# Kernel optimization log

Measured on AMD Instinct MI355X. Metric: run time of the kernel, lower is better.

## Reference

```python
import jax, jax.numpy as jnp
import numpy as np

B, S, E, H = 4, 1024, 1024, 16
HD = E // H  # head_dim = 64
MAX_SEQ = 1024  # rel positions span [-(MAX_SEQ-1), MAX_SEQ-1]


def setup_inputs() -> dict:
    key = jax.random.key(0)
    ks = jax.random.split(key, 12)
    std_e = 1.0 / np.sqrt(E)
    std_h = 1.0 / np.sqrt(HD)
    inp = {
        "x": jax.random.normal(ks[0], (B, S, E), dtype=jnp.float32),
        # torch nn.Linear weights are [out, in]; y = x @ W.T + b
        "Wq": jax.random.uniform(ks[1], (E, E), jnp.float32, -std_e, std_e),
        "bq": jax.random.uniform(ks[2], (E,), jnp.float32, -std_e, std_e),
        "Wk": jax.random.uniform(ks[3], (E, E), jnp.float32, -std_e, std_e),
        "bk": jax.random.uniform(ks[4], (E,), jnp.float32, -std_e, std_e),
        "Wv": jax.random.uniform(ks[5], (E, E), jnp.float32, -std_e, std_e),
        "bv": jax.random.uniform(ks[6], (E,), jnp.float32, -std_e, std_e),
        "Wo": jax.random.uniform(ks[7], (E, E), jnp.float32, -std_e, std_e),
        "bo": jax.random.uniform(ks[8], (E,), jnp.float32, -std_e, std_e),
        # pos_key_proj: Linear(head_dim, head_dim, bias=False)
        "Wp": jax.random.uniform(ks[9], (HD, HD), jnp.float32, -std_h, std_h),
        # learned relative position table [2*max_seq_len-1, head_dim]
        "rel_table": jax.random.normal(ks[10], (2 * MAX_SEQ - 1, HD), dtype=jnp.float32),
    }
    return inp


def _rel_shift(pos_scores):
    # pos_scores: [B, H, S, 2S-1] -> [B, H, S, S]
    # result[..., i, j] = pos_scores[..., i, (S-1) - i + j]
    s = pos_scores.shape[-2]
    idx = (s - 1) - jnp.arange(s)[:, None] + jnp.arange(s)[None, :]  # [S, S]
    return jnp.take_along_axis(pos_scores, idx[None, None, :, :], axis=-1)


def reference(x, Wq, bq, Wk, bk, Wv, bv, Wo, bo, Wp, rel_table):
    scale = 1.0 / np.sqrt(HD)
    Q = (x @ Wq.T + bq).reshape(B, S, H, HD).transpose(0, 2, 1, 3)  # [B,H,S,HD]
    K = (x @ Wk.T + bk).reshape(B, S, H, HD).transpose(0, 2, 1, 3)
    V = (x @ Wv.T + bv).reshape(B, S, H, HD).transpose(0, 2, 1, 3)

    # rel_pos_encoding(S): slice centered at MAX_SEQ-1 covering 2S-1 positions
    center = MAX_SEQ - 1
    rel_emb = rel_table[center - (S - 1): center + S]  # [2S-1, HD]
    rel_key = rel_emb @ Wp.T                            # [2S-1, HD]

    content = jnp.einsum("bhqd,bhkd->bhqk", Q, K) * scale       # [B,H,S,S]
    pos = jnp.einsum("bhqd,pd->bhqp", Q, rel_key) * scale       # [B,H,S,2S-1]
    scores = content + _rel_shift(pos)                          # [B,H,S,S]

    probs = jax.nn.softmax(scores, axis=-1)
    ctx = jnp.einsum("bhqk,bhkd->bhqd", probs, V)               # [B,H,S,HD]
    ctx = ctx.transpose(0, 2, 1, 3).reshape(B, S, E)
    return ctx @ Wo.T + bo
```

## Files before the change

### kernel.cpp

```cpp
#include <hip/hip_runtime.h>
#include <hip/hip_bf16.h>

#define B_   4
#define S_   1024
#define E_   1024
#define H_   16
#define HD_  64

typedef float  f32x4  __attribute__((ext_vector_type(4)));
typedef short  bf16x8 __attribute__((ext_vector_type(8)));
typedef short  bf16x4 __attribute__((ext_vector_type(4)));

__device__ __forceinline__ float bf2f(short u) {
  union { unsigned int i; float f; } v;
  v.i = ((unsigned int)(unsigned short)u) << 16;
  return v.f;
}
__device__ __forceinline__ short f2bf(float f) {
  unsigned int x = __float_as_uint(f);
  x = x + 0x7fffu + ((x >> 16) & 1u);
  return (short)(x >> 16);
}
__device__ __forceinline__ bf16x8 ld_cvt8(const float* __restrict__ p) {
  const f32x4 a = *(const f32x4*)p;
  const f32x4 b = *(const f32x4*)(p + 4);
  bf16x8 r;
  r[0] = f2bf(a[0]); r[1] = f2bf(a[1]); r[2] = f2bf(a[2]); r[3] = f2bf(a[3]);
  r[4] = f2bf(b[0]); r[5] = f2bf(b[1]); r[6] = f2bf(b[2]); r[7] = f2bf(b[3]);
  return r;
}

__device__ __forceinline__ void gload_lds16(const short* g, short* l) {
  __builtin_amdgcn_global_load_lds(
      (const __attribute__((address_space(1))) void*)g,
      (__attribute__((address_space(3))) void*)l, 16, 0, 0);
}

__global__ __launch_bounds__(256) void cvt_f32_bf16(
    const float* __restrict__ src, short* __restrict__ dst, int n)
{
  const int i = (blockIdx.x * 256 + threadIdx.x) * 4;
  if (i < n) {
    const f32x4 v = *(const f32x4*)(src + i);
    bf16x4 o;
    o[0] = f2bf(v[0]); o[1] = f2bf(v[1]); o[2] = f2bf(v[2]); o[3] = f2bf(v[3]);
    *(bf16x4*)(dst + i) = o;
  }
}

__global__ __launch_bounds__(256) void cvt3_f32_bf16(
    const float* __restrict__ s0, const float* __restrict__ s1,
    const float* __restrict__ s2, short* __restrict__ dst, int n)
{
  const float* src = (blockIdx.z == 0) ? s0 : (blockIdx.z == 1) ? s1 : s2;
  short* d = dst + (size_t)blockIdx.z * n;
  const int i = (blockIdx.x * 256 + threadIdx.x) * 4;
  if (i < n) {
    const f32x4 v = *(const f32x4*)(src + i);
    bf16x4 o;
    o[0] = f2bf(v[0]); o[1] = f2bf(v[1]); o[2] = f2bf(v[2]); o[3] = f2bf(v[3]);
    *(bf16x4*)(d + i) = o;
  }
}

template<int TM, int AF32, int OUTF32>
__global__ __launch_bounds__(256) void gemm_bt(
    const void* __restrict__ Av,
    const short* __restrict__ W0, const short* __restrict__ W1, const short* __restrict__ W2,
    const float* __restrict__ b0, const float* __restrict__ b1, const float* __restrict__ b2,
    void* __restrict__ C0v, void* __restrict__ C1v, void* __restrict__ C2v, int vz)
{
  constexpr int NJ = (TM == 128) ? 4 : 2;
  __shared__ short As[TM * 32];
  __shared__ short Bs[128 * 32];

  const int tid  = threadIdx.x;
  const int lane = tid & 63;
  const int wave = tid >> 6;
  const int quad = lane >> 4;
  const int l15  = lane & 15;
  const int wmb  = (TM == 128) ? (wave >> 1) * 64 : 0;
  const int wnb  = (TM == 128) ? (wave & 1) * 64 : wave * 32;
  const int m0   = blockIdx.y * TM;
  const int n0   = blockIdx.x * 128;
  const int z    = blockIdx.z;

  const short* W  = (z == 0) ? W0 : (z == 1) ? W1 : W2;
  const float* bb = (z == 0) ? b0 : (z == 1) ? b1 : b2;
  void*        Cv = (z == 0) ? C0v : (z == 1) ? C1v : C2v;

  const int trow = tid >> 2;
  const int tc   = tid & 3;

  f32x4 acc[4][NJ] = {};

  for (int k0 = 0; k0 < E_; k0 += 32) {
    if (AF32) {
      const float* A = (const float*)Av;
#pragma unroll
      for (int n = 0; n < TM / 64; ++n) {
        const int row = trow + n * 64;
        const int pc  = tc ^ ((row >> 1) & 3);
        *(bf16x8*)&As[row * 32 + pc * 8] = ld_cvt8(A + (size_t)(m0 + row) * E_ + k0 + tc * 8);
      }
    } else {
      const short* A = (const short*)Av;
#pragma unroll
      for (int n = 0; n < TM / 64; ++n) {
        const int row  = trow + n * 64;
        const int srcc = tc ^ ((row >> 1) & 3);
        gload_lds16(A + (size_t)(m0 + row) * E_ + k0 + srcc * 8, &As[n * 2048 + tid * 8]);
      }
    }
#pragma unroll
    for (int n = 0; n < 2; ++n) {
      const int row  = trow + n * 64;
      const int srcc = tc ^ ((row >> 1) & 3);
      gload_lds16(W + (size_t)(n0 + row) * E_ + k0 + srcc * 8, &Bs[n * 2048 + tid * 8]);
    }
    __syncthreads();

    bf16x8 af[4], bfr[NJ];
#pragma unroll
    for (int i = 0; i < 4; ++i) {
      const int row = wmb + i * 16 + l15;
      const int pc  = quad ^ ((row >> 1) & 3);
      af[i] = *(bf16x8*)&As[row * 32 + pc * 8];
    }
#pragma unroll
    for (int j = 0; j < NJ; ++j) {
      const int row = wnb + j * 16 + l15;
      const int pc  = quad ^ ((row >> 1) & 3);
      bfr[j] = *(bf16x8*)&Bs[row * 32 + pc * 8];
    }
#pragma unroll
    for (int i = 0; i < 4; ++i)
#pragma unroll
      for (int j = 0; j < NJ; ++j)
        acc[i][j] = __builtin_amdgcn_mfma_f32_16x16x32_bf16(af[i], bfr[j], acc[i][j], 0, 0, 0);
    __syncthreads();
  }

  if (TM == 128 && z == vz) {
    const int mtb = m0 + wmb;
    const int bq  = mtb >> 10;
    const int kt  = (mtb >> 6) & 15;
    short* Cs = (short*)Cv;
#pragma unroll
    for (int j = 0; j < NJ; ++j) {
      const int n = n0 + wnb + j * 16 + l15;
      const float bv = bb[n];
      const int h = (n >> 6) & 15;
      const int d = n & 63;
      bf16x8 lo, hi;
#pragma unroll
      for (int e = 0; e < 8; ++e) {
        lo[e] = f2bf(acc[e & 3][j][e >> 2] + bv);
        hi[e] = f2bf(acc[e & 3][j][(e >> 2) + 2] + bv);
      }
      const size_t off = ((size_t)((bq * 16 + h) * 64 + d)) * 1024 + kt * 64 + quad * 16;
      *(bf16x8*)(Cs + off)     = lo;
      *(bf16x8*)(Cs + off + 8) = hi;
    }
  } else {
#pragma unroll
    for (int j = 0; j < NJ; ++j) {
      const int n = n0 + wnb + j * 16 + l15;
      const float bv = bb[n];
#pragma unroll
      for (int i = 0; i < 4; ++i) {
        const int m = m0 + wmb + i * 16 + quad * 4;
#pragma unroll
        for (int r = 0; r < 4; ++r) {
          const float v = acc[i][j][r] + bv;
          if (OUTF32) ((float*)Cv)[(size_t)(m + r) * E_ + n] = v;
          else        ((short*)Cv)[(size_t)(m + r) * E_ + n] = f2bf(v);
        }
      }
    }
  }
}

__global__ __launch_bounds__(64) void relkey_kernel(
    const float* __restrict__ rel, const float* __restrict__ Wp, short* __restrict__ RKw)
{
  const int p = blockIdx.x;
  const int d = threadIdx.x;
  __shared__ float rs[64];
  rs[d] = rel[p * 64 + d];
  __syncthreads();
  float acc = 0.f;
#pragma unroll
  for (int e = 0; e < 64; ++e)
    acc += rs[e] * Wp[d * 64 + e];
  RKw[p * 64 + d] = f2bf(acc);
}

__global__ __launch_bounds__(512, 4) void attn_kernel(
    const short* __restrict__ Qw, const short* __restrict__ Kw,
    const short* __restrict__ Vtg, const short* __restrict__ RKw,
    short* __restrict__ Cw)
{
  __shared__ short Ks[64][72];
  __shared__ short Vt[64][72];
  __shared__ short RKs[192][72];
  __shared__ short Ps[8][16][72];

  const int tid  = threadIdx.x;
  const int lane = tid & 63;
  const int wv   = tid >> 6;
  const int quad = lane >> 4;
  const int l15  = lane & 15;
  const int q0   = blockIdx.x * 128;
  const int h    = blockIdx.y;
  const int b    = blockIdx.z;
  const int bh   = b * 16 + h;
  const int qw0  = q0 + wv * 16;
  const int jb   = 112 - 16 * wv;
  const int pbase0 = S_ - 128 - q0;

  bf16x8 qf[2];
  {
    const size_t base = (size_t)(b * S_ + qw0 + l15) * E_ + h * HD_ + quad * 8;
    qf[0] = *(const bf16x8*)(Qw + base);
    qf[1] = *(const bf16x8*)(Qw + base + 32);
  }

  f32x4 oacc[4] = {};
  float lsum[4] = {0.f, 0.f, 0.f, 0.f};

  const float fs = 0.125f * 1.44269504088896340736f;

  const int sr  = tid >> 3;
  const int sc8 = (tid & 7) * 8;

#pragma unroll 1
  for (int kt = 0; kt < 16; ++kt) {
    const int k0 = kt * 64;

    *(bf16x8*)&Ks[sr][sc8] =
        *(const bf16x8*)(Kw + (size_t)(b * S_ + k0 + sr) * E_ + h * HD_ + sc8);
    *(bf16x8*)&Vt[sr][sc8] =
        *(const bf16x8*)(Vtg + (size_t)(bh * 64 + sr) * 1024 + k0 + sc8);
    if (kt == 0) {
#pragma unroll
      for (int jj = 0; jj < 3; ++jj) {
        const int c = tid + jj * 512;
        const int row = c >> 3, ch = (c & 7) * 8;
        int p = pbase0 + row; p = (p > 2046) ? 2046 : p;
        *(bf16x8*)&RKs[row][ch] = *(const bf16x8*)(RKw + (size_t)p * 64 + ch);
      }
    } else {
      const int phys0 = 64 * ((kt + 2) % 3);
      int p = pbase0 + 64 * kt + 128 + sr; p = (p > 2046) ? 2046 : p;
      *(bf16x8*)&RKs[phys0 + sr][sc8] = *(const bf16x8*)(RKw + (size_t)p * 64 + sc8);
    }
    __syncthreads();

    const int s64 = 64 * (kt % 3);

    f32x4 sc[4] = {};
#pragma unroll
    for (int s = 0; s < 2; ++s) {
#pragma unroll
      for (int kk = 0; kk < 4; ++kk) {
        bf16x8 bf = *(bf16x8*)&Ks[kk*16 + l15][s*32 + quad*8];
        sc[kk] = __builtin_amdgcn_mfma_f32_16x16x32_bf16(qf[s], bf, sc[kk], 0, 0, 0);
      }
    }

    f32x4 ta[5] = {};
#pragma unroll
    for (int jt = 0; jt < 5; ++jt) {
      int phys = s64 + jb + jt * 16;
      if (phys >= 192) phys -= 192;
#pragma unroll
      for (int s = 0; s < 2; ++s) {
        bf16x8 bf = *(bf16x8*)&RKs[phys + l15][s*32 + quad*8];
        ta[jt] = __builtin_amdgcn_mfma_f32_16x16x32_bf16(qf[s], bf, ta[jt], 0, 0, 0);
      }
    }

    float p[4][4];
#pragma unroll
    for (int r = 0; r < 4; ++r) {
      const int i16 = quad*4 + r;
      const int d   = 15 + l15 - i16;
      const int srcLane = (quad << 4) | (d & 15);
      float sj[5];
#pragma unroll
      for (int jt = 0; jt < 5; ++jt) sj[jt] = __shfl(ta[jt][r], srcLane, 64);
      const bool hi = (d >= 16);
#pragma unroll
      for (int kk = 0; kk < 4; ++kk) {
        const float t = hi ? sj[kk+1] : sj[kk];
        const float sv = fminf((sc[kk][r] + t) * fs, 108.f);
        const float pv = exp2f(sv - 12.f);
        p[kk][r] = pv;
        lsum[r] += pv;
      }
    }

#pragma unroll
    for (int r = 0; r < 4; ++r) {
      bf16x4 pw;
      pw[0] = f2bf(p[0][r]); pw[1] = f2bf(p[1][r]);
      pw[2] = f2bf(p[2][r]); pw[3] = f2bf(p[3][r]);
      *(bf16x4*)&Ps[wv][quad*4 + r][l15*4] = pw;
    }

#pragma unroll
    for (int ks = 0; ks < 2; ++ks) {
      bf16x8 pa = *(bf16x8*)&Ps[wv][l15][ks*32 + quad*8];
#pragma unroll
      for (int dt = 0; dt < 4; ++dt) {
        bf16x8 vb = *(bf16x8*)&Vt[dt*16 + l15][ks*32 + quad*8];
        oacc[dt] = __builtin_amdgcn_mfma_f32_16x16x32_bf16(pa, vb, oacc[dt], 0, 0, 0);
      }
    }
    __syncthreads();
  }

#pragma unroll
  for (int off = 1; off <= 8; off <<= 1)
#pragma unroll
    for (int r = 0; r < 4; ++r)
      lsum[r] += __shfl_xor(lsum[r], off, 64);

#pragma unroll
  for (int r = 0; r < 4; ++r) {
    const float inv = 1.0f / lsum[r];
    const size_t row = (size_t)(b * S_ + qw0 + quad*4 + r) * E_ + h * HD_;
#pragma unroll
    for (int dt = 0; dt < 4; ++dt)
      Cw[row + dt*16 + l15] = f2bf(oacc[dt][r] * inv);
  }
}

__global__ void fill_kernel(float* __restrict__ out, int n, float val) {
  for (int i = blockIdx.x * blockDim.x + threadIdx.x; i < n; i += gridDim.x * blockDim.x)
    out[i] = val;
}

extern "C" void kernel_launch(void* const* d_in, const int* in_sizes, int n_in,
                              void* d_out, int out_size, void* d_ws, size_t ws_size,
                              hipStream_t stream)
{
  const size_t WS_NEEDED = 33816448;
  if (ws_size < WS_NEEDED) {
    fill_kernel<<<1024, 256, 0, stream>>>((float*)d_out, out_size, 0.25f);
    return;
  }
  if (n_in != 11 || in_sizes[10] != 2047 * 64) {
    fill_kernel<<<1024, 256, 0, stream>>>((float*)d_out, out_size, 0.75f);
    return;
  }

  const float* x   = (const float*)d_in[0];
  const float* Wq  = (const float*)d_in[1];
  const float* bq  = (const float*)d_in[2];
  const float* Wk  = (const float*)d_in[3];
  const float* bk  = (const float*)d_in[4];
  const float* Wv  = (const float*)d_in[5];
  const float* bv  = (const float*)d_in[6];
  const float* Wo  = (const float*)d_in[7];
  const float* bo  = (const float*)d_in[8];
  const float* Wp  = (const float*)d_in[9];
  const float* rel = (const float*)d_in[10];

  char* ws = (char*)d_ws;
  short* Qws = (short*)(ws);
  short* Kws = (short*)(ws + 8388608);
  short* Vtg = (short*)(ws + 16777216);
  short* WB  = (short*)(ws + 25165824);
  short* ctx = (short*)(ws + 25165824);
  short* WoB = (short*)(ws + 8388608);
  short* RKw = (short*)(ws + 33554432);

  const int NW = E_ * E_;

  cvt3_f32_bf16<<<dim3(NW / 1024, 1, 3), dim3(256), 0, stream>>>(Wq, Wk, Wv, WB, NW);

  gemm_bt<128, 1, 0><<<dim3(8, 32, 3), dim3(256), 0, stream>>>(
      x, WB, WB + NW, WB + 2 * NW, bq, bk, bv, Qws, Kws, Vtg, 2);

  relkey_kernel<<<dim3(2047), dim3(64), 0, stream>>>(rel, Wp, RKw);

  attn_kernel<<<dim3(8, 16, 4), dim3(512), 0, stream>>>(Qws, Kws, Vtg, RKw, ctx);

  cvt_f32_bf16<<<dim3(NW / 1024), dim3(256), 0, stream>>>(Wo, WoB, NW);

  gemm_bt<64, 0, 1><<<dim3(8, 64, 1), dim3(256), 0, stream>>>(
      ctx, WoB, WoB, WoB, bo, bo, bo, d_out, d_out, d_out, -1);
}
```

Baseline: 292.4 us.

## Pre-convert x to bf16 for async LDS loads and use MFMA for rel-key projection

The activation x is now converted to bf16 in the same launch as the Q/K/V weights, with d_out serving as scratch. This lets the QKV GEMM load A tiles with direct global-to-LDS loads instead of per-thread fp32 load, convert and LDS store, at the cost of an extra full write and read of x in bf16. The rel-key projection is also rewritten from a scalar per-thread dot product over 2047 small blocks to a 32-block MFMA kernel. The FP32 A path in the GEMM is removed.

Measured after the change: 273.6 us. 1.07x faster.

```diff
diff --git a/kernel.cpp b/kernel.cpp
--- a/kernel.cpp
+++ b/kernel.cpp
@@ -48,24 +48,27 @@
   }
 }
 
-__global__ __launch_bounds__(256) void cvt3_f32_bf16(
-    const float* __restrict__ s0, const float* __restrict__ s1,
-    const float* __restrict__ s2, short* __restrict__ dst, int n)
-{
-  const float* src = (blockIdx.z == 0) ? s0 : (blockIdx.z == 1) ? s1 : s2;
-  short* d = dst + (size_t)blockIdx.z * n;
+__global__ __launch_bounds__(256) void cvt7_f32_bf16(
+    const float* __restrict__ w0, const float* __restrict__ w1,
+    const float* __restrict__ w2, const float* __restrict__ x,
+    short* __restrict__ WB, short* __restrict__ xbf)
+{
+  const int NW = E_ * E_;
+  const int y = blockIdx.y;
+  const float* src;
+  short* dst;
+  if (y < 3) { src = (y == 0) ? w0 : (y == 1) ? w1 : w2; dst = WB + (size_t)y * NW; }
+  else       { src = x + (size_t)(y - 3) * NW;           dst = xbf + (size_t)(y - 3) * NW; }
   const int i = (blockIdx.x * 256 + threadIdx.x) * 4;
-  if (i < n) {
-    const f32x4 v = *(const f32x4*)(src + i);
-    bf16x4 o;
-    o[0] = f2bf(v[0]); o[1] = f2bf(v[1]); o[2] = f2bf(v[2]); o[3] = f2bf(v[3]);
-    *(bf16x4*)(d + i) = o;
-  }
-}
-
-template<int TM, int AF32, int OUTF32>
+  const f32x4 v = *(const f32x4*)(src + i);
+  bf16x4 o;
+  o[0] = f2bf(v[0]); o[1] = f2bf(v[1]); o[2] = f2bf(v[2]); o[3] = f2bf(v[3]);
+  *(bf16x4*)(dst + i) = o;
+}
+
+template<int TM, int OUTF32>
 __global__ __launch_bounds__(256) void gemm_bt(
-    const void* __restrict__ Av,
+    const short* __restrict__ A,
     const short* __restrict__ W0, const short* __restrict__ W1, const short* __restrict__ W2,
     const float* __restrict__ b0, const float* __restrict__ b1, const float* __restrict__ b2,
     void* __restrict__ C0v, void* __restrict__ C1v, void* __restrict__ C2v, int vz)
@@ -95,22 +98,11 @@
   f32x4 acc[4][NJ] = {};
 
   for (int k0 = 0; k0 < E_; k0 += 32) {
-    if (AF32) {
-      const float* A = (const float*)Av;
-#pragma unroll
-      for (int n = 0; n < TM / 64; ++n) {
-        const int row = trow + n * 64;
-        const int pc  = tc ^ ((row >> 1) & 3);
-        *(bf16x8*)&As[row * 32 + pc * 8] = ld_cvt8(A + (size_t)(m0 + row) * E_ + k0 + tc * 8);
-      }
-    } else {
-      const short* A = (const short*)Av;
-#pragma unroll
-      for (int n = 0; n < TM / 64; ++n) {
-        const int row  = trow + n * 64;
-        const int srcc = tc ^ ((row >> 1) & 3);
-        gload_lds16(A + (size_t)(m0 + row) * E_ + k0 + srcc * 8, &As[n * 2048 + tid * 8]);
-      }
+#pragma unroll
+    for (int n = 0; n < TM / 64; ++n) {
+      const int row  = trow + n * 64;
+      const int srcc = tc ^ ((row >> 1) & 3);
+      gload_lds16(A + (size_t)(m0 + row) * E_ + k0 + srcc * 8, &As[n * 2048 + tid * 8]);
     }
 #pragma unroll
     for (int n = 0; n < 2; ++n) {
@@ -181,19 +173,38 @@
   }
 }
 
-__global__ __launch_bounds__(64) void relkey_kernel(
+__global__ __launch_bounds__(256) void relkey_mfma(
     const float* __restrict__ rel, const float* __restrict__ Wp, short* __restrict__ RKw)
 {
-  const int p = blockIdx.x;
-  const int d = threadIdx.x;
-  __shared__ float rs[64];
-  rs[d] = rel[p * 64 + d];
-  __syncthreads();
-  float acc = 0.f;
-#pragma unroll
-  for (int e = 0; e < 64; ++e)
-    acc += rs[e] * Wp[d * 64 + e];
-  RKw[p * 64 + d] = f2bf(acc);
+  const int tid  = threadIdx.x;
+  const int lane = tid & 63;
+  const int wv   = tid >> 6;
+  const int quad = lane >> 4;
+  const int l15  = lane & 15;
+  const int p0   = blockIdx.x * 64 + wv * 16;
+
+  bf16x8 af[2];
+  {
+    int prow = p0 + l15; if (prow > 2046) prow = 2046;
+    const float* ap = rel + (size_t)prow * 64 + quad * 8;
+    af[0] = ld_cvt8(ap);
+    af[1] = ld_cvt8(ap + 32);
+  }
+  f32x4 acc[4] = {};
+#pragma unroll
+  for (int nt = 0; nt < 4; ++nt) {
+    const float* bp = Wp + (size_t)(nt * 16 + l15) * 64 + quad * 8;
+    acc[nt] = __builtin_amdgcn_mfma_f32_16x16x32_bf16(af[0], ld_cvt8(bp),      acc[nt], 0, 0, 0);
+    acc[nt] = __builtin_amdgcn_mfma_f32_16x16x32_bf16(af[1], ld_cvt8(bp + 32), acc[nt], 0, 0, 0);
+  }
+#pragma unroll
+  for (int r = 0; r < 4; ++r) {
+    const int p = p0 + quad * 4 + r;
+    if (p < 2047)
+#pragma unroll
+      for (int nt = 0; nt < 4; ++nt)
+        RKw[(size_t)p * 64 + nt * 16 + l15] = f2bf(acc[nt][r]);
+  }
 }
 
 __global__ __launch_bounds__(512, 4) void attn_kernel(
@@ -376,20 +387,21 @@
   short* ctx = (short*)(ws + 25165824);
   short* WoB = (short*)(ws + 8388608);
   short* RKw = (short*)(ws + 33554432);
+  short* xbf = (short*)d_out;
 
   const int NW = E_ * E_;
 
-  cvt3_f32_bf16<<<dim3(NW / 1024, 1, 3), dim3(256), 0, stream>>>(Wq, Wk, Wv, WB, NW);
-
-  gemm_bt<128, 1, 0><<<dim3(8, 32, 3), dim3(256), 0, stream>>>(
-      x, WB, WB + NW, WB + 2 * NW, bq, bk, bv, Qws, Kws, Vtg, 2);
-
-  relkey_kernel<<<dim3(2047), dim3(64), 0, stream>>>(rel, Wp, RKw);
+  cvt7_f32_bf16<<<dim3(1024, 7), dim3(256), 0, stream>>>(Wq, Wk, Wv, x, WB, xbf);
+
+  gemm_bt<128, 0><<<dim3(8, 32, 3), dim3(256), 0, stream>>>(
+      xbf, WB, WB + NW, WB + 2 * NW, bq, bk, bv, Qws, Kws, Vtg, 2);
+
+  relkey_mfma<<<dim3(32), dim3(256), 0, stream>>>(rel, Wp, RKw);
 
   attn_kernel<<<dim3(8, 16, 4), dim3(512), 0, stream>>>(Qws, Kws, Vtg, RKw, ctx);
 
   cvt_f32_bf16<<<dim3(NW / 1024), dim3(256), 0, stream>>>(Wo, WoB, NW);
 
-  gemm_bt<64, 0, 1><<<dim3(8, 64, 1), dim3(256), 0, stream>>>(
+  gemm_bt<64, 1><<<dim3(8, 64, 1), dim3(256), 0, stream>>>(
       ctx, WoB, WoB, WoB, bo, bo, bo, d_out, d_out, d_out, -1);
 }
```
